# Optimization experiments

Measured on AMD Instinct MI355X. Metric: run time of the kernel, lower is better.

## Reference

```python
import jax, jax.numpy as jnp
import numpy as np

D_MODEL = 2048
B, T, N = 4, 2048, 512


def setup_inputs() -> dict:
    key = jax.random.key(0)
    k1, k2, k3, k4, k5 = jax.random.split(key, 5)
    x = jax.random.normal(k1, (B, T, D_MODEL), dtype=jnp.float32)
    h_stack = jax.random.normal(k2, (B, N, D_MODEL), dtype=jnp.float32)
    m_stack = jax.random.normal(k3, (B, N, D_MODEL), dtype=jnp.float32)
    m_current = jax.random.normal(k4, (B, T, D_MODEL), dtype=jnp.float32)
    # block-causal visibility: position t can see cache entry j iff j <= t*N/T
    causal_mask = jnp.arange(N)[None, :] <= (jnp.arange(T)[:, None] * N // T)
    # learned projection, torch Linear stores weight as (out, in): u = x @ W.T
    W_u = jax.random.normal(k5, (D_MODEL, D_MODEL), dtype=jnp.float32) * (1.0 / np.sqrt(D_MODEL))
    return {"x": x, "h_stack": h_stack, "m_stack": m_stack,
            "m_current": m_current, "causal_mask": causal_mask, "W_u": W_u}


def reference(x, h_stack, m_stack, m_current, causal_mask, W_u):
    D = x.shape[-1]
    n = m_stack.shape[1]
    scale = 1.0 / jnp.sqrt(jnp.asarray(D, x.dtype))
    u = jnp.einsum('btd,ed->bte', x, W_u)                      # Linear(no bias): x @ W.T
    scores_cached = jnp.einsum('btd,bnd->btn', u, m_stack) * scale
    neg_inf = jnp.asarray(-jnp.inf, scores_cached.dtype)
    scores_cached = jnp.where(causal_mask[None, :, :], scores_cached, neg_inf)
    scores_current = jnp.sum(u * m_current, axis=-1, keepdims=True) * scale  # (B,T,1)
    all_scores = jnp.concatenate([scores_cached, scores_current], axis=-1)   # (B,T,N+1)
    attn_weights = jax.nn.softmax(all_scores, axis=-1)
    gates_cached = attn_weights[:, :, :n]
    gate_current = attn_weights[:, :, n:]
    h_retrieved = jnp.einsum('btn,bnd->btd', gates_cached, h_stack)
    return h_retrieved, gate_current, attn_weights
```

## Files before the change

kernel.cpp:

```cpp
#include <hip/hip_runtime.h>

#define D_MODEL 2048
#define B_SZ 4
#define T_SZ 2048
#define N_SZ 512

typedef __bf16 bf16x8 __attribute__((ext_vector_type(8)));
typedef float f32x4 __attribute__((ext_vector_type(4)));
typedef ushort u16x8 __attribute__((ext_vector_type(8)));

__device__ __forceinline__ ushort f2bf(float f) {
  unsigned u = __float_as_uint(f);
  unsigned r = (u + 0x7fffu + ((u >> 16) & 1u)) >> 16;
  return (ushort)r;
}
__device__ __forceinline__ float bflo(unsigned w) { return __uint_as_float(w << 16); }
__device__ __forceinline__ float bfhi(unsigned w) { return __uint_as_float(w & 0xffff0000u); }

__device__ __forceinline__ void async_ld16(const ushort* g, ushort* l) {
  __builtin_amdgcn_global_load_lds(
      (const __attribute__((address_space(1))) void*)g,
      (__attribute__((address_space(3))) void*)l, 16, 0, 0);
}

__global__ __launch_bounds__(256) void conv_bf16(const float* __restrict__ src,
                                                 ushort* __restrict__ dst) {
  const long i = ((long)blockIdx.x * 256 + threadIdx.x) * 8;
  float4 a = *(const float4*)(src + i);
  float4 b = *(const float4*)(src + i + 4);
  u16x8 o;
  o[0] = f2bf(a.x); o[1] = f2bf(a.y); o[2] = f2bf(a.z); o[3] = f2bf(a.w);
  o[4] = f2bf(b.x); o[5] = f2bf(b.y); o[6] = f2bf(b.z); o[7] = f2bf(b.w);
  *(u16x8*)(dst + i) = o;
}

__global__ __launch_bounds__(256) void transpose_conv(const float* __restrict__ src,
                                                      ushort* __restrict__ dst) {
  __shared__ ushort tile[32][33];
  const int b = blockIdx.z;
  const int n0 = blockIdx.x * 32, d0 = blockIdx.y * 32;
  const int tx = threadIdx.x, ty = threadIdx.y;
  const float* s = src + (long)b * N_SZ * D_MODEL;
  ushort* d = dst + (long)b * D_MODEL * N_SZ;
#pragma unroll
  for (int r = 0; r < 4; r++)
    tile[ty + r * 8][tx] = f2bf(s[(long)(n0 + ty + r * 8) * D_MODEL + d0 + tx]);
  __syncthreads();
#pragma unroll
  for (int r = 0; r < 4; r++)
    d[(long)(d0 + ty + r * 8) * N_SZ + n0 + tx] = tile[tx][ty + r * 8];
}

template <int MASKMODE, bool OUT_BF16>
__global__ __launch_bounds__(256) void gemm_bt(const ushort* __restrict__ A,
                                               const ushort* __restrict__ Bt,
                                               void* __restrict__ Cv, int M, int N, int K,
                                               long sA, long sB, long sC, float scale) {
  __shared__ __align__(16) ushort sa[128 * 32];
  __shared__ __align__(16) ushort sb[128 * 32];
  const int bz = blockIdx.z;
  const int row0 = blockIdx.y * 128;
  const int col0 = blockIdx.x * 128;
  if (MASKMODE == 1 && col0 > ((row0 + 127) >> 2)) return;
  int Kend = K;
  if (MASKMODE == 2) {
    int kl = ((row0 + 127) >> 2) + 1;
    Kend = min(K, (kl + 31) & ~31);
  }
  const ushort* Ab = A + (long)bz * sA;
  const ushort* Bb = Bt + (long)bz * sB;

  const int tid = threadIdx.x;
  const int w = tid >> 6, lane = tid & 63;
  const int wr = w >> 1, wc = w & 1;
  const int quad = lane >> 4, l16 = lane & 15;

  f32x4 acc[4][4];
#pragma unroll
  for (int i = 0; i < 4; i++)
#pragma unroll
    for (int j = 0; j < 4; j++) acc[i][j] = (f32x4){0.f, 0.f, 0.f, 0.f};

  const int ch = w * 2;
  const int srow = ch * 16 + (lane >> 2);
  const int scol = (lane & 3) * 8;
  ushort* ldsA0 = sa + ch * 512;
  ushort* ldsA1 = sa + ch * 512 + 512;
  ushort* ldsB0 = sb + ch * 512;
  ushort* ldsB1 = sb + ch * 512 + 512;
  const ushort* gA0 = Ab + (long)(row0 + srow) * K + scol;
  const ushort* gA1 = Ab + (long)(row0 + srow + 16) * K + scol;
  const ushort* gB0 = Bb + (long)(col0 + srow) * K + scol;
  const ushort* gB1 = Bb + (long)(col0 + srow + 16) * K + scol;

  for (int k0 = 0; k0 < Kend; k0 += 32) {
    async_ld16(gA0 + k0, ldsA0);
    async_ld16(gA1 + k0, ldsA1);
    async_ld16(gB0 + k0, ldsB0);
    async_ld16(gB1 + k0, ldsB1);
    __syncthreads();
    bf16x8 af[4], bfr[4];
#pragma unroll
    for (int i = 0; i < 4; i++) {
      af[i] = *(const bf16x8*)(sa + (wr * 64 + i * 16 + l16) * 32 + quad * 8);
      bfr[i] = *(const bf16x8*)(sb + (wc * 64 + i * 16 + l16) * 32 + quad * 8);
    }
#pragma unroll
    for (int i = 0; i < 4; i++)
#pragma unroll
      for (int j = 0; j < 4; j++)
        acc[i][j] = __builtin_amdgcn_mfma_f32_16x16x32_bf16(af[i], bfr[j], acc[i][j], 0, 0, 0);
    __syncthreads();
  }

#pragma unroll
  for (int i = 0; i < 4; i++) {
    const int rb = row0 + wr * 64 + i * 16 + quad * 4;
#pragma unroll
    for (int j = 0; j < 4; j++) {
      const int c = col0 + wc * 64 + j * 16 + l16;
#pragma unroll
      for (int r = 0; r < 4; r++) {
        float v = acc[i][j][r] * scale;
        long off = (long)bz * sC + (long)(rb + r) * N + c;
        if (OUT_BF16)
          ((ushort*)Cv)[off] = f2bf(v);
        else
          ((float*)Cv)[off] = v;
      }
    }
  }
}

__global__ __launch_bounds__(256) void softmax_gate(const ushort* __restrict__ u_bf,
                                                    const float* __restrict__ m_cur,
                                                    const float* __restrict__ scores,
                                                    float* __restrict__ out_gc,
                                                    float* __restrict__ out_attn,
                                                    ushort* __restrict__ gates_bf) {
  __shared__ float red[256];
  const int bt = blockIdx.x;
  const int t = bt & (T_SZ - 1);
  const int tid = threadIdx.x;
  const ushort* urow = u_bf + (long)bt * D_MODEL;
  const float* mrow = m_cur + (long)bt * D_MODEL;
  uint4 uv = *(const uint4*)(urow + tid * 8);
  float4 m0 = *(const float4*)(mrow + tid * 8);
  float4 m1 = *(const float4*)(mrow + tid * 8 + 4);
  float part = bflo(uv.x) * m0.x + bfhi(uv.x) * m0.y + bflo(uv.y) * m0.z + bfhi(uv.y) * m0.w +
               bflo(uv.z) * m1.x + bfhi(uv.z) * m1.y + bflo(uv.w) * m1.z + bfhi(uv.w) * m1.w;
  red[tid] = part;
  __syncthreads();
  for (int s = 128; s > 0; s >>= 1) {
    if (tid < s) red[tid] += red[tid + s];
    __syncthreads();
  }
  const float curs = red[0] * 0.022097086912079608f;
  __syncthreads();

  const int nmax = t >> 2;
  const float* srow = scores + (long)bt * N_SZ;
  float lmax = curs;
  for (int n = tid; n <= nmax; n += 256) lmax = fmaxf(lmax, srow[n]);
  red[tid] = lmax;
  __syncthreads();
  for (int s = 128; s > 0; s >>= 1) {
    if (tid < s) red[tid] = fmaxf(red[tid], red[tid + s]);
    __syncthreads();
  }
  const float M = red[0];
  __syncthreads();
  float lsum = (tid == 0) ? __expf(curs - M) : 0.f;
  for (int n = tid; n <= nmax; n += 256) lsum += __expf(srow[n] - M);
  red[tid] = lsum;
  __syncthreads();
  for (int s = 128; s > 0; s >>= 1) {
    if (tid < s) red[tid] += red[tid + s];
    __syncthreads();
  }
  const float inv = 1.f / red[0];

  float* arow = out_attn + (long)bt * (N_SZ + 1);
  ushort* grow = gates_bf + (long)bt * N_SZ;
  for (int n = tid; n < N_SZ; n += 256) {
    float wgt = (n <= nmax) ? __expf(srow[n] - M) * inv : 0.f;
    arow[n] = wgt;
    grow[n] = f2bf(wgt);
  }
  if (tid == 0) {
    float g = __expf(curs - M) * inv;
    arow[N_SZ] = g;
    out_gc[bt] = g;
  }
}

extern "C" void kernel_launch(void* const* d_in, const int* in_sizes, int n_in,
                              void* d_out, int out_size, void* d_ws, size_t ws_size,
                              hipStream_t stream) {
  const float* x = (const float*)d_in[0];
  const float* h_stack = (const float*)d_in[1];
  const float* m_stack = (const float*)d_in[2];
  const float* m_cur = (const float*)d_in[3];
  const float* W = (const float*)d_in[5];

  float* out = (float*)d_out;
  float* out_h = out;
  float* out_gc = out + (long)B_SZ * T_SZ * D_MODEL;
  float* out_attn = out_gc + B_SZ * T_SZ;

  char* ws = (char*)d_ws;
  ushort* x_bf = (ushort*)ws;
  ushort* u_bf = x_bf + 16777216;
  ushort* W_bf = u_bf + 16777216;
  ushort* ms_bf = W_bf + 4194304;
  ushort* gates = ms_bf + 4194304;
  ushort* hsT = gates + 4194304;
  float* scores = (float*)(hsT + 4194304);

  conv_bf16<<<16777216 / 2048, 256, 0, stream>>>(x, x_bf);
  conv_bf16<<<4194304 / 2048, 256, 0, stream>>>(W, W_bf);
  conv_bf16<<<4194304 / 2048, 256, 0, stream>>>(m_stack, ms_bf);
  transpose_conv<<<dim3(N_SZ / 32, D_MODEL / 32, B_SZ), dim3(32, 8), 0, stream>>>(h_stack, hsT);

  gemm_bt<0, true><<<dim3(D_MODEL / 128, (B_SZ * T_SZ) / 128, 1), 256, 0, stream>>>(
      x_bf, W_bf, u_bf, B_SZ * T_SZ, D_MODEL, D_MODEL, 0, 0, 0, 1.0f);

  gemm_bt<1, false><<<dim3(N_SZ / 128, T_SZ / 128, B_SZ), 256, 0, stream>>>(
      u_bf, ms_bf, scores, T_SZ, N_SZ, D_MODEL, (long)T_SZ * D_MODEL, (long)N_SZ * D_MODEL,
      (long)T_SZ * N_SZ, 0.022097086912079608f);

  softmax_gate<<<B_SZ * T_SZ, 256, 0, stream>>>(u_bf, m_cur, scores, out_gc, out_attn, gates);

  gemm_bt<2, false><<<dim3(D_MODEL / 128, T_SZ / 128, B_SZ), 256, 0, stream>>>(
      gates, hsT, out_h, T_SZ, D_MODEL, N_SZ, (long)T_SZ * N_SZ, (long)D_MODEL * N_SZ,
      (long)T_SZ * D_MODEL, 1.0f);
}
```

Baseline: 408.7 us.

## Merge conversions, shrink score GEMM tile, and use one wavefront per softmax row

Three bf16 conversion launches become a single kernel that picks its source by block index. The score GEMM gains a templated row-tile size and runs with 64-row tiles, so it launches more blocks and the causal skip is finer. Softmax now gives each row to one wavefront, reduces with shuffles instead of LDS and barriers, and keeps the scores in registers so exp is computed once. The aim is to cut launch overhead and synchronisation and improve occupancy, at the cost of smaller per-block reuse in the score GEMM.

```diff
diff --git a/kernel.cpp b/kernel.cpp
--- a/kernel.cpp
+++ b/kernel.cpp
@@ -23,9 +23,20 @@
       (__attribute__((address_space(3))) void*)l, 16, 0, 0);
 }
 
-__global__ __launch_bounds__(256) void conv_bf16(const float* __restrict__ src,
-                                                 ushort* __restrict__ dst) {
-  const long i = ((long)blockIdx.x * 256 + threadIdx.x) * 8;
+__global__ __launch_bounds__(256) void conv_all(const float* __restrict__ x,
+                                                const float* __restrict__ W,
+                                                const float* __restrict__ ms,
+                                                ushort* __restrict__ x_bf,
+                                                ushort* __restrict__ W_bf,
+                                                ushort* __restrict__ ms_bf) {
+  const int bid = blockIdx.x;
+  const float* src;
+  ushort* dst;
+  long blk;
+  if (bid < 8192) { src = x; dst = x_bf; blk = bid; }
+  else if (bid < 10240) { src = W; dst = W_bf; blk = bid - 8192; }
+  else { src = ms; dst = ms_bf; blk = bid - 10240; }
+  const long i = (blk * 256 + threadIdx.x) * 8;
   float4 a = *(const float4*)(src + i);
   float4 b = *(const float4*)(src + i + 4);
   u16x8 o;
@@ -51,20 +62,24 @@
     d[(long)(d0 + ty + r * 8) * N_SZ + n0 + tx] = tile[tx][ty + r * 8];
 }
 
-template <int MASKMODE, bool OUT_BF16>
+template <int TM, int MASKMODE, bool OUT_BF16>
 __global__ __launch_bounds__(256) void gemm_bt(const ushort* __restrict__ A,
                                                const ushort* __restrict__ Bt,
-                                               void* __restrict__ Cv, int M, int N, int K,
+                                               void* __restrict__ Cv, int N, int K,
                                                long sA, long sB, long sC, float scale) {
-  __shared__ __align__(16) ushort sa[128 * 32];
+  constexpr int NA = TM / 16;
+  constexpr int NCH = NA + 8;
+  constexpr int NC = NCH / 4;
+  constexpr int NI = TM / 32;
+  __shared__ __align__(16) ushort sa[TM * 32];
   __shared__ __align__(16) ushort sb[128 * 32];
   const int bz = blockIdx.z;
-  const int row0 = blockIdx.y * 128;
+  const int row0 = blockIdx.y * TM;
   const int col0 = blockIdx.x * 128;
-  if (MASKMODE == 1 && col0 > ((row0 + 127) >> 2)) return;
+  if (MASKMODE == 1 && col0 > ((row0 + TM - 1) >> 2)) return;
   int Kend = K;
   if (MASKMODE == 2) {
-    int kl = ((row0 + 127) >> 2) + 1;
+    int kl = ((row0 + TM - 1) >> 2) + 1;
     Kend = min(K, (kl + 31) & ~31);
   }
   const ushort* Ab = A + (long)bz * sA;
@@ -75,38 +90,41 @@
   const int wr = w >> 1, wc = w & 1;
   const int quad = lane >> 4, l16 = lane & 15;
 
-  f32x4 acc[4][4];
-#pragma unroll
-  for (int i = 0; i < 4; i++)
+  f32x4 acc[NI][4];
+#pragma unroll
+  for (int i = 0; i < NI; i++)
 #pragma unroll
     for (int j = 0; j < 4; j++) acc[i][j] = (f32x4){0.f, 0.f, 0.f, 0.f};
 
-  const int ch = w * 2;
-  const int srow = ch * 16 + (lane >> 2);
-  const int scol = (lane & 3) * 8;
-  ushort* ldsA0 = sa + ch * 512;
-  ushort* ldsA1 = sa + ch * 512 + 512;
-  ushort* ldsB0 = sb + ch * 512;
-  ushort* ldsB1 = sb + ch * 512 + 512;
-  const ushort* gA0 = Ab + (long)(row0 + srow) * K + scol;
-  const ushort* gA1 = Ab + (long)(row0 + srow + 16) * K + scol;
-  const ushort* gB0 = Bb + (long)(col0 + srow) * K + scol;
-  const ushort* gB1 = Bb + (long)(col0 + srow + 16) * K + scol;
+  const int lrow = lane >> 2;
+  const int lcol = (lane & 3) * 8;
+  const ushort* gsrc[NC];
+  ushort* ldst[NC];
+#pragma unroll
+  for (int t = 0; t < NC; t++) {
+    const int c = w * NC + t;
+    if (c < NA) {
+      ldst[t] = sa + c * 512;
+      gsrc[t] = Ab + (long)(row0 + c * 16 + lrow) * K + lcol;
+    } else {
+      ldst[t] = sb + (c - NA) * 512;
+      gsrc[t] = Bb + (long)(col0 + (c - NA) * 16 + lrow) * K + lcol;
+    }
+  }
 
   for (int k0 = 0; k0 < Kend; k0 += 32) {
-    async_ld16(gA0 + k0, ldsA0);
-    async_ld16(gA1 + k0, ldsA1);
-    async_ld16(gB0 + k0, ldsB0);
-    async_ld16(gB1 + k0, ldsB1);
+#pragma unroll
+    for (int t = 0; t < NC; t++) async_ld16(gsrc[t] + k0, ldst[t]);
     __syncthreads();
-    bf16x8 af[4], bfr[4];
-#pragma unroll
-    for (int i = 0; i < 4; i++) {
-      af[i] = *(const bf16x8*)(sa + (wr * 64 + i * 16 + l16) * 32 + quad * 8);
-      bfr[i] = *(const bf16x8*)(sb + (wc * 64 + i * 16 + l16) * 32 + quad * 8);
-    }
-#pragma unroll
-    for (int i = 0; i < 4; i++)
+    bf16x8 af[NI], bfr[4];
+#pragma unroll
+    for (int i = 0; i < NI; i++)
+      af[i] = *(const bf16x8*)(sa + (wr * (TM / 2) + i * 16 + l16) * 32 + quad * 8);
+#pragma unroll
+    for (int j = 0; j < 4; j++)
+      bfr[j] = *(const bf16x8*)(sb + (wc * 64 + j * 16 + l16) * 32 + quad * 8);
+#pragma unroll
+    for (int i = 0; i < NI; i++)
 #pragma unroll
       for (int j = 0; j < 4; j++)
         acc[i][j] = __builtin_amdgcn_mfma_f32_16x16x32_bf16(af[i], bfr[j], acc[i][j], 0, 0, 0);
@@ -114,8 +132,8 @@
   }
 
 #pragma unroll
-  for (int i = 0; i < 4; i++) {
-    const int rb = row0 + wr * 64 + i * 16 + quad * 4;
+  for (int i = 0; i < NI; i++) {
+    const int rb = row0 + wr * (TM / 2) + i * 16 + quad * 4;
 #pragma unroll
     for (int j = 0; j < 4; j++) {
       const int c = col0 + wc * 64 + j * 16 + l16;
@@ -138,57 +156,60 @@
                                                     float* __restrict__ out_gc,
                                                     float* __restrict__ out_attn,
                                                     ushort* __restrict__ gates_bf) {
-  __shared__ float red[256];
-  const int bt = blockIdx.x;
+  const int wv = threadIdx.x >> 6, lane = threadIdx.x & 63;
+  const int bt = blockIdx.x * 4 + wv;
   const int t = bt & (T_SZ - 1);
-  const int tid = threadIdx.x;
   const ushort* urow = u_bf + (long)bt * D_MODEL;
   const float* mrow = m_cur + (long)bt * D_MODEL;
-  uint4 uv = *(const uint4*)(urow + tid * 8);
-  float4 m0 = *(const float4*)(mrow + tid * 8);
-  float4 m1 = *(const float4*)(mrow + tid * 8 + 4);
-  float part = bflo(uv.x) * m0.x + bfhi(uv.x) * m0.y + bflo(uv.y) * m0.z + bfhi(uv.y) * m0.w +
-               bflo(uv.z) * m1.x + bfhi(uv.z) * m1.y + bflo(uv.w) * m1.z + bfhi(uv.w) * m1.w;
-  red[tid] = part;
-  __syncthreads();
-  for (int s = 128; s > 0; s >>= 1) {
-    if (tid < s) red[tid] += red[tid + s];
-    __syncthreads();
-  }
-  const float curs = red[0] * 0.022097086912079608f;
-  __syncthreads();
+
+  float part = 0.f;
+#pragma unroll
+  for (int c = 0; c < 4; c++) {
+    uint4 uv = *(const uint4*)(urow + c * 512 + lane * 8);
+    float4 m0 = *(const float4*)(mrow + c * 512 + lane * 8);
+    float4 m1 = *(const float4*)(mrow + c * 512 + lane * 8 + 4);
+    part += bflo(uv.x) * m0.x + bfhi(uv.x) * m0.y + bflo(uv.y) * m0.z + bfhi(uv.y) * m0.w +
+            bflo(uv.z) * m1.x + bfhi(uv.z) * m1.y + bflo(uv.w) * m1.z + bfhi(uv.w) * m1.w;
+  }
+#pragma unroll
+  for (int m = 32; m; m >>= 1) part += __shfl_xor(part, m, 64);
+  const float curs = part * 0.022097086912079608f;
 
   const int nmax = t >> 2;
   const float* srow = scores + (long)bt * N_SZ;
+  float sc[8];
   float lmax = curs;
-  for (int n = tid; n <= nmax; n += 256) lmax = fmaxf(lmax, srow[n]);
-  red[tid] = lmax;
-  __syncthreads();
-  for (int s = 128; s > 0; s >>= 1) {
-    if (tid < s) red[tid] = fmaxf(red[tid], red[tid + s]);
-    __syncthreads();
-  }
-  const float M = red[0];
-  __syncthreads();
-  float lsum = (tid == 0) ? __expf(curs - M) : 0.f;
-  for (int n = tid; n <= nmax; n += 256) lsum += __expf(srow[n] - M);
-  red[tid] = lsum;
-  __syncthreads();
-  for (int s = 128; s > 0; s >>= 1) {
-    if (tid < s) red[tid] += red[tid + s];
-    __syncthreads();
-  }
-  const float inv = 1.f / red[0];
+#pragma unroll
+  for (int k = 0; k < 8; k++) {
+    const int n = k * 64 + lane;
+    sc[k] = srow[n];
+    if (n <= nmax) lmax = fmaxf(lmax, sc[k]);
+  }
+#pragma unroll
+  for (int m = 32; m; m >>= 1) lmax = fmaxf(lmax, __shfl_xor(lmax, m, 64));
+
+  float lsum = (lane == 0) ? __expf(curs - lmax) : 0.f;
+#pragma unroll
+  for (int k = 0; k < 8; k++) {
+    const int n = k * 64 + lane;
+    sc[k] = (n <= nmax) ? __expf(sc[k] - lmax) : 0.f;
+    lsum += sc[k];
+  }
+#pragma unroll
+  for (int m = 32; m; m >>= 1) lsum += __shfl_xor(lsum, m, 64);
+  const float inv = 1.f / lsum;
 
   float* arow = out_attn + (long)bt * (N_SZ + 1);
   ushort* grow = gates_bf + (long)bt * N_SZ;
-  for (int n = tid; n < N_SZ; n += 256) {
-    float wgt = (n <= nmax) ? __expf(srow[n] - M) * inv : 0.f;
+#pragma unroll
+  for (int k = 0; k < 8; k++) {
+    const int n = k * 64 + lane;
+    const float wgt = sc[k] * inv;
     arow[n] = wgt;
     grow[n] = f2bf(wgt);
   }
-  if (tid == 0) {
-    float g = __expf(curs - M) * inv;
+  if (lane == 0) {
+    const float g = __expf(curs - lmax) * inv;
     arow[N_SZ] = g;
     out_gc[bt] = g;
   }
@@ -217,21 +238,20 @@
   ushort* hsT = gates + 4194304;
   float* scores = (float*)(hsT + 4194304);
 
-  conv_bf16<<<16777216 / 2048, 256, 0, stream>>>(x, x_bf);
-  conv_bf16<<<4194304 / 2048, 256, 0, stream>>>(W, W_bf);
-  conv_bf16<<<4194304 / 2048, 256, 0, stream>>>(m_stack, ms_bf);
+  conv_all<<<12288, 256, 0, stream>>>(x, W, m_stack, x_bf, W_bf, ms_bf);
   transpose_conv<<<dim3(N_SZ / 32, D_MODEL / 32, B_SZ), dim3(32, 8), 0, stream>>>(h_stack, hsT);
 
-  gemm_bt<0, true><<<dim3(D_MODEL / 128, (B_SZ * T_SZ) / 128, 1), 256, 0, stream>>>(
-      x_bf, W_bf, u_bf, B_SZ * T_SZ, D_MODEL, D_MODEL, 0, 0, 0, 1.0f);
-
-  gemm_bt<1, false><<<dim3(N_SZ / 128, T_SZ / 128, B_SZ), 256, 0, stream>>>(
-      u_bf, ms_bf, scores, T_SZ, N_SZ, D_MODEL, (long)T_SZ * D_MODEL, (long)N_SZ * D_MODEL,
+  gemm_bt<128, 0, true><<<dim3(D_MODEL / 128, (B_SZ * T_SZ) / 128, 1), 256, 0, stream>>>(
+      x_bf, W_bf, u_bf, D_MODEL, D_MODEL, 0, 0, 0, 1.0f);
+
+  gemm_bt<64, 1, false><<<dim3(N_SZ / 128, T_SZ / 64, B_SZ), 256, 0, stream>>>(
+      u_bf, ms_bf, scores, N_SZ, D_MODEL, (long)T_SZ * D_MODEL, (long)N_SZ * D_MODEL,
       (long)T_SZ * N_SZ, 0.022097086912079608f);
 
-  softmax_gate<<<B_SZ * T_SZ, 256, 0, stream>>>(u_bf, m_cur, scores, out_gc, out_attn, gates);
-
-  gemm_bt<2, false><<<dim3(D_MODEL / 128, T_SZ / 128, B_SZ), 256, 0, stream>>>(
-      gates, hsT, out_h, T_SZ, D_MODEL, N_SZ, (long)T_SZ * N_SZ, (long)D_MODEL * N_SZ,
+  softmax_gate<<<(B_SZ * T_SZ) / 4, 256, 0, stream>>>(u_bf, m_cur, scores, out_gc, out_attn,
+                                                      gates);
+
+  gemm_bt<128, 2, false><<<dim3(D_MODEL / 128, T_SZ / 128, B_SZ), 256, 0, stream>>>(
+      gates, hsT, out_h, D_MODEL, N_SZ, (long)T_SZ * N_SZ, (long)D_MODEL * N_SZ,
       (long)T_SZ * D_MODEL, 1.0f);
 }
```

Result: faster. 394.8 us (-3.4%).
